# Optimization experiments

Measured on AMD Instinct MI355X. Metric: run time of the kernel, lower is better.

The kernel has to match this reference:

```python
import jax, jax.numpy as jnp
import numpy as np

K_HOPS = 4  # matches init kwarg K


def setup_inputs() -> dict:
    key = jax.random.key(0)
    ks = jax.random.split(key, 6)
    B, N, Fin, Fout = 32, 128, 64, 64
    x = jax.random.normal(ks[0], (B, N, Fin), dtype=jnp.float32)
    P = jax.random.normal(ks[1], (N, N), dtype=jnp.float32)
    Bb = jax.random.normal(ks[2], (N, 1), dtype=jnp.float32)
    Q = jax.random.normal(ks[3], (Fin, Fin), dtype=jnp.float32)
    T = jax.random.normal(ks[4], (Fin, N * Fin), dtype=jnp.float32)
    U = jax.random.normal(ks[5], (Fin, Fout), dtype=jnp.float32)
    return {"x": x, "P": P, "Bb": Bb, "Q": Q, "T": T, "U": U}


def reference(x, P, Bb, Q, T, U):
    B, N, Fin = x.shape
    # adjacency generation: O = P x + b, G = relu((O Q) T)
    O = jnp.matmul(P, x) + Bb                      # (B, N, Fin)
    G = jax.nn.relu(jnp.matmul(jnp.matmul(O, Q), T))  # (B, N, N*Fin)
    G = G.reshape(B, N, N, Fin).transpose(0, 3, 1, 2)  # (B, Fin, N, N)
    # degree normalization: A = diag(1/sqrt(colsum)) G diag(1/sqrt(rowsum))
    Dii = jnp.sqrt(jnp.sum(G, axis=-2))            # (B, Fin, N) column sums
    Djj = jnp.sqrt(jnp.sum(G, axis=-1))            # (B, Fin, N) row sums
    A = G / Dii[..., :, None] / Djj[..., None, :]  # (B, Fin, N, N)
    # K-hop power series: Asum = I + A + ... + A^{K-1}
    AA = jnp.broadcast_to(jnp.eye(N, dtype=x.dtype), A.shape)
    Asum = jnp.zeros_like(A)
    for _ in range(K_HOPS - 1):
        Asum = Asum + AA
        AA = jnp.matmul(A, AA)
    Asum = Asum + AA
    # propagate each feature channel: X[b,n,f] = sum_m Asum[b,f,n,m] x[b,m,f]
    Xf = jnp.einsum('bfnm,bmf->bnf', Asum, x)      # (B, N, Fin)
    return jnp.matmul(Xf, U)                       # (B, N, Fout)
```

## Files before the change

kernel.cpp:

```cpp
#include <hip/hip_runtime.h>


typedef __attribute__((ext_vector_type(8))) short short8v;
typedef __attribute__((ext_vector_type(4))) float f32x4;

#define WS_THE 0u
#define WS_TLE (1u << 20)
#define WS_OQH (2u << 20)
#define WS_OQL ((2u << 20) + (512u << 10))
#define WS_XFT (3u << 20)

__device__ __forceinline__ void split_bf16(float a, unsigned& hi, unsigned& lo) {
  unsigned ha = __float_as_uint(a) & 0xffff0000u;
  float d = a - __uint_as_float(ha);
  unsigned la = __float_as_uint(d) & 0xffff0000u;
  hi = ha; lo = la;
}

__global__ __launch_bounds__(256) void iag_kpre(
    const float* __restrict__ T, const float* __restrict__ x,
    const float* __restrict__ P, const float* __restrict__ Q,
    const float* __restrict__ Bb,
    unsigned short* __restrict__ The, unsigned short* __restrict__ Tle,
    unsigned short* __restrict__ OQh, unsigned short* __restrict__ OQl) {
  __shared__ __align__(16) char smem[73856];
  int bi = blockIdx.x, tid = threadIdx.x;

  if (bi < 64) {
    float* tile = (float*)smem;
    int m0 = bi * 2;
    for (int idx = tid; idx < 8192; idx += 256) {
      int k = idx >> 7, j = idx & 127;
      tile[k * 129 + j] = T[k * 8192 + m0 * 64 + j];
    }
    __syncthreads();
    int p = tid >> 1, kc = (tid & 1) * 32;
    int fj = p & 63, ml = p >> 6;
    int j = ml * 64 + fj;
    unsigned hw[16], lw[16];
#pragma unroll
    for (int kk = 0; kk < 32; kk += 2) {
      float a0 = tile[(kc + kk) * 129 + j];
      float a1 = tile[(kc + kk + 1) * 129 + j];
      unsigned h0, l0, h1, l1;
      split_bf16(a0, h0, l0);
      split_bf16(a1, h1, l1);
      hw[kk >> 1] = (h0 >> 16) | h1;
      lw[kk >> 1] = (l0 >> 16) | l1;
    }
    uint4* dh = (uint4*)(The + fj * 8192 + (m0 + ml) * 64 + kc);
    uint4* dl = (uint4*)(Tle + fj * 8192 + (m0 + ml) * 64 + kc);
#pragma unroll
    for (int i = 0; i < 4; ++i) {
      dh[i] = make_uint4(hw[4 * i], hw[4 * i + 1], hw[4 * i + 2], hw[4 * i + 3]);
      dl[i] = make_uint4(lw[4 * i], lw[4 * i + 1], lw[4 * i + 2], lw[4 * i + 3]);
    }
  } else {
    float* x_s   = (float*)smem;
    float* ptile = x_s + 128 * 64;
    float* Q_s   = ptile + 32 * 129;
    float* OcT   = Q_s + 64 * 64;
    int jb = bi - 64;
    int b = jb >> 2, r0 = (jb & 3) * 32;

    const float4* xg = (const float4*)(x + b * 8192);
    float4* xs4 = (float4*)x_s;
    for (int idx = tid; idx < 2048; idx += 256) xs4[idx] = xg[idx];
    for (int idx = tid; idx < 4096; idx += 256) {
      int nl = idx >> 7, m = idx & 127;
      ptile[nl * 129 + m] = P[(r0 + nl) * 128 + m];
    }
    const float4* qg = (const float4*)Q;
    float4* qs4 = (float4*)Q_s;
    for (int idx = tid; idx < 1024; idx += 256) qs4[idx] = qg[idx];
    __syncthreads();

    {
      int nl = tid & 31, k0 = (tid >> 5) * 8;
      float bias = Bb[r0 + nl];
      float a[8];
#pragma unroll
      for (int j = 0; j < 8; ++j) a[j] = bias;
#pragma unroll 4
      for (int m = 0; m < 128; ++m) {
        float p = ptile[nl * 129 + m];
        float4 x0 = xs4[m * 16 + (k0 >> 2)];
        float4 x1 = xs4[m * 16 + (k0 >> 2) + 1];
        a[0] += p * x0.x; a[1] += p * x0.y; a[2] += p * x0.z; a[3] += p * x0.w;
        a[4] += p * x1.x; a[5] += p * x1.y; a[6] += p * x1.z; a[7] += p * x1.w;
      }
#pragma unroll
      for (int j = 0; j < 8; ++j) OcT[(k0 + j) * 32 + nl] = a[j];
    }
    __syncthreads();
    {
      int nl = tid >> 3, j0 = (tid & 7) * 8;
      float c[8];
#pragma unroll
      for (int i = 0; i < 8; ++i) c[i] = 0.f;
      const float4* q4 = (const float4*)Q_s;
#pragma unroll 4
      for (int k = 0; k < 64; ++k) {
        float o = OcT[k * 32 + nl];
        float4 q0 = q4[k * 16 + (j0 >> 2)];
        float4 q1 = q4[k * 16 + (j0 >> 2) + 1];
        c[0] += o * q0.x; c[1] += o * q0.y; c[2] += o * q0.z; c[3] += o * q0.w;
        c[4] += o * q1.x; c[5] += o * q1.y; c[6] += o * q1.z; c[7] += o * q1.w;
      }
      unsigned hw[4], lw[4];
#pragma unroll
      for (int j = 0; j < 8; j += 2) {
        unsigned h0, l0, h1, l1;
        split_bf16(c[j], h0, l0);
        split_bf16(c[j + 1], h1, l1);
        hw[j >> 1] = (h0 >> 16) | h1;
        lw[j >> 1] = (l0 >> 16) | l1;
      }
      int n = r0 + nl;
      *(uint4*)(OQh + b * 8192 + n * 64 + j0) = make_uint4(hw[0], hw[1], hw[2], hw[3]);
      *(uint4*)(OQl + b * 8192 + n * 64 + j0) = make_uint4(lw[0], lw[1], lw[2], lw[3]);
    }
  }
}

__global__ __launch_bounds__(256, 4) void iag_k2_graph(
    const unsigned short* __restrict__ OQh, const unsigned short* __restrict__ OQl,
    const unsigned short* __restrict__ The, const unsigned short* __restrict__ Tle,
    const float* __restrict__ x, float* __restrict__ Xft) {
  __shared__ float red[4 * 128];
  __shared__ float invc[128], invr[128];
  __shared__ float wvb[2][128];
  int f = blockIdx.x, b = blockIdx.y, tid = threadIdx.x;

  if (tid < 128) wvb[0][tid] = x[b * 8192 + tid * 64 + f];

  int lane = tid & 63, w = tid >> 6;
  int li = lane & 15, lk = lane >> 4;

  const unsigned short* Abh = OQh + b * 8192;
  const unsigned short* Abl = OQl + b * 8192;
  const unsigned short* Bbh = The + f * 8192;
  const unsigned short* Bbl = Tle + f * 8192;

  short8v ah[2][2], al[2][2];
#pragma unroll
  for (int nt = 0; nt < 2; ++nt)
#pragma unroll
    for (int kh = 0; kh < 2; ++kh) {
      int off = (w * 32 + nt * 16 + li) * 64 + kh * 32 + lk * 8;
      ah[nt][kh] = *(const short8v*)(Abh + off);
      al[nt][kh] = *(const short8v*)(Abl + off);
    }

  f32x4 acc[2][8];
#pragma unroll
  for (int nt = 0; nt < 2; ++nt)
#pragma unroll
    for (int mt = 0; mt < 8; ++mt) acc[nt][mt] = (f32x4){0.f, 0.f, 0.f, 0.f};

#pragma unroll
  for (int mt = 0; mt < 8; ++mt) {
    int off = (mt * 16 + li) * 64 + lk * 8;
    short8v bh0 = *(const short8v*)(Bbh + off);
    short8v bh1 = *(const short8v*)(Bbh + off + 32);
    short8v bl0 = *(const short8v*)(Bbl + off);
    short8v bl1 = *(const short8v*)(Bbl + off + 32);
#pragma unroll
    for (int nt = 0; nt < 2; ++nt) {
      f32x4 a = acc[nt][mt];
      a = __builtin_amdgcn_mfma_f32_16x16x32_bf16(ah[nt][0], bh0, a, 0, 0, 0);
      a = __builtin_amdgcn_mfma_f32_16x16x32_bf16(ah[nt][1], bh1, a, 0, 0, 0);
      a = __builtin_amdgcn_mfma_f32_16x16x32_bf16(ah[nt][0], bl0, a, 0, 0, 0);
      a = __builtin_amdgcn_mfma_f32_16x16x32_bf16(ah[nt][1], bl1, a, 0, 0, 0);
      a = __builtin_amdgcn_mfma_f32_16x16x32_bf16(al[nt][0], bh0, a, 0, 0, 0);
      a = __builtin_amdgcn_mfma_f32_16x16x32_bf16(al[nt][1], bh1, a, 0, 0, 0);
      acc[nt][mt] = a;
    }
  }

#pragma unroll
  for (int nt = 0; nt < 2; ++nt)
#pragma unroll
    for (int mt = 0; mt < 8; ++mt)
#pragma unroll
      for (int r = 0; r < 4; ++r) acc[nt][mt][r] = fmaxf(acc[nt][mt][r], 0.f);

#pragma unroll
  for (int mt = 0; mt < 8; ++mt) {
    float cs = 0.f;
#pragma unroll
    for (int nt = 0; nt < 2; ++nt)
#pragma unroll
      for (int r = 0; r < 4; ++r) cs += acc[nt][mt][r];
    cs += __shfl_xor(cs, 16);
    cs += __shfl_xor(cs, 32);
    if (lk == 0) red[w * 128 + mt * 16 + li] = cs;
  }
  {
    float rs[2][4];
#pragma unroll
    for (int nt = 0; nt < 2; ++nt)
#pragma unroll
      for (int r = 0; r < 4; ++r) {
        float s = 0.f;
#pragma unroll
        for (int mt = 0; mt < 8; ++mt) s += acc[nt][mt][r];
        rs[nt][r] = s;
      }
#pragma unroll
    for (int d = 1; d <= 8; d <<= 1)
#pragma unroll
      for (int nt = 0; nt < 2; ++nt)
#pragma unroll
        for (int r = 0; r < 4; ++r) rs[nt][r] += __shfl_xor(rs[nt][r], d);
    if (li == 0) {
#pragma unroll
      for (int nt = 0; nt < 2; ++nt)
#pragma unroll
        for (int r = 0; r < 4; ++r)
          invr[w * 32 + nt * 16 + lk * 4 + r] = rs[nt][r];
    }
  }
  __syncthreads();
  if (tid < 128) {
    float csum = red[tid] + red[128 + tid] + red[256 + tid] + red[384 + tid];
    invc[tid] = 1.0f / sqrtf(csum);
    invr[tid] = 1.0f / sqrtf(invr[tid]);
  }
  __syncthreads();

  {
    float icf[2][4], irf[8];
#pragma unroll
    for (int nt = 0; nt < 2; ++nt)
#pragma unroll
      for (int r = 0; r < 4; ++r) icf[nt][r] = invc[w * 32 + nt * 16 + lk * 4 + r];
#pragma unroll
    for (int mt = 0; mt < 8; ++mt) irf[mt] = invr[mt * 16 + li];
#pragma unroll
    for (int nt = 0; nt < 2; ++nt)
#pragma unroll
      for (int mt = 0; mt < 8; ++mt)
#pragma unroll
        for (int r = 0; r < 4; ++r) acc[nt][mt][r] *= icf[nt][r] * irf[mt];
  }

  float sv[2][4];
#pragma unroll
  for (int nt = 0; nt < 2; ++nt)
#pragma unroll
    for (int r = 0; r < 4; ++r) sv[nt][r] = wvb[0][w * 32 + nt * 16 + lk * 4 + r];
  int cur = 0;
  for (int h = 0; h < 3; ++h) {
    float wr[8];
#pragma unroll
    for (int mt = 0; mt < 8; ++mt) wr[mt] = wvb[cur][mt * 16 + li];
    float p[2][4];
#pragma unroll
    for (int nt = 0; nt < 2; ++nt)
#pragma unroll
      for (int r = 0; r < 4; ++r) {
        float s = 0.f;
#pragma unroll
        for (int mt = 0; mt < 8; ++mt) s += acc[nt][mt][r] * wr[mt];
        p[nt][r] = s;
      }
#pragma unroll
    for (int d = 1; d <= 8; d <<= 1)
#pragma unroll
      for (int nt = 0; nt < 2; ++nt)
#pragma unroll
        for (int r = 0; r < 4; ++r) p[nt][r] += __shfl_xor(p[nt][r], d);
#pragma unroll
    for (int nt = 0; nt < 2; ++nt)
#pragma unroll
      for (int r = 0; r < 4; ++r) sv[nt][r] += p[nt][r];
    if (li == 0) {
#pragma unroll
      for (int nt = 0; nt < 2; ++nt)
#pragma unroll
        for (int r = 0; r < 4; ++r)
          wvb[cur ^ 1][w * 32 + nt * 16 + lk * 4 + r] = p[nt][r];
    }
    __syncthreads();
    cur ^= 1;
  }
  if (li == 0) {
#pragma unroll
    for (int nt = 0; nt < 2; ++nt)
#pragma unroll
      for (int r = 0; r < 4; ++r)
        Xft[(b * 64 + f) * 128 + w * 32 + nt * 16 + lk * 4 + r] = sv[nt][r];
  }
}

__global__ __launch_bounds__(256) void iag_k3_out(
    const float* __restrict__ Xft, const float* __restrict__ U,
    float* __restrict__ out) {
  __shared__ float Xf_s[64 * 36];
  __shared__ __align__(16) float U_s[64 * 64];
  int b = blockIdx.y, n0 = blockIdx.x * 32, tid = threadIdx.x;
  for (int c = tid; c < 512; c += 256) {
    int ff = c >> 3, s = c & 7;
    float4 v = *(const float4*)(Xft + (b * 64 + ff) * 128 + n0 + s * 4);
    *(float4*)(Xf_s + ff * 36 + s * 4) = v;
  }
  const float4* ug = (const float4*)U;
  float4* us = (float4*)U_s;
  for (int c = tid; c < 1024; c += 256) us[c] = ug[c];
  __syncthreads();

  int j0 = (tid & 15) * 4, nl0 = (tid >> 4) * 2;
  float a0[4] = {0.f, 0.f, 0.f, 0.f}, a1[4] = {0.f, 0.f, 0.f, 0.f};
  const float4* u4 = (const float4*)U_s;
#pragma unroll 4
  for (int ff = 0; ff < 64; ++ff) {
    float4 u = u4[ff * 16 + (j0 >> 2)];
    float xa = Xf_s[ff * 36 + nl0];
    float xb = Xf_s[ff * 36 + nl0 + 1];
    a0[0] += xa * u.x; a0[1] += xa * u.y; a0[2] += xa * u.z; a0[3] += xa * u.w;
    a1[0] += xb * u.x; a1[1] += xb * u.y; a1[2] += xb * u.z; a1[3] += xb * u.w;
  }
  *(float4*)(out + b * 8192 + (n0 + nl0) * 64 + j0) =
      make_float4(a0[0], a0[1], a0[2], a0[3]);
  *(float4*)(out + b * 8192 + (n0 + nl0 + 1) * 64 + j0) =
      make_float4(a1[0], a1[1], a1[2], a1[3]);
}

extern "C" void kernel_launch(void* const* d_in, const int* in_sizes, int n_in,
                              void* d_out, int out_size, void* d_ws, size_t ws_size,
                              hipStream_t stream) {
  const float* x  = (const float*)d_in[0];
  const float* P  = (const float*)d_in[1];
  const float* Bb = (const float*)d_in[2];
  const float* Q  = (const float*)d_in[3];
  const float* T  = (const float*)d_in[4];
  const float* U  = (const float*)d_in[5];
  char* wsb = (char*)d_ws;
  unsigned short* The = (unsigned short*)(wsb + WS_THE);
  unsigned short* Tle = (unsigned short*)(wsb + WS_TLE);
  unsigned short* OQh = (unsigned short*)(wsb + WS_OQH);
  unsigned short* OQl = (unsigned short*)(wsb + WS_OQL);
  float* Xft = (float*)(wsb + WS_XFT);

  iag_kpre<<<192, 256, 0, stream>>>(T, x, P, Q, Bb, The, Tle, OQh, OQl);
  iag_k2_graph<<<dim3(64, 32), 256, 0, stream>>>(OQh, OQl, The, Tle, x, Xft);
  iag_k3_out<<<dim3(4, 32), 256, 0, stream>>>(Xft, U, (float*)d_out);
}
```

Measured before the change: 124.2 us.

## Pre-transpose x for coalesced loads and double-buffer B fragments in graph kernel

Adds 64 extra blocks to the preprocessing kernel that transpose x per batch into a feature-major buffer. The graph kernel can then load its per-feature x vector contiguously instead of with a stride of 64 floats. The graph kernel also prefetches the next mt tile's T hi/lo fragments into a second register slot while the MFMAs for the current tile run. The occupancy hint drops from 4 to 3 blocks per CU to make room for the extra registers. The cost is one more workspace buffer, extra transpose work in the pre-kernel, and possibly lower occupancy.

Result: no change. 125.6 us (+1.1%).

```diff
diff --git a/kernel.cpp b/kernel.cpp
--- a/kernel.cpp
+++ b/kernel.cpp
@@ -9,6 +9,7 @@
 #define WS_OQH (2u << 20)
 #define WS_OQL ((2u << 20) + (512u << 10))
 #define WS_XFT (3u << 20)
+#define WS_XT  (4u << 20)
 
 __device__ __forceinline__ void split_bf16(float a, unsigned& hi, unsigned& lo) {
   unsigned ha = __float_as_uint(a) & 0xffff0000u;
@@ -22,7 +23,8 @@
     const float* __restrict__ P, const float* __restrict__ Q,
     const float* __restrict__ Bb,
     unsigned short* __restrict__ The, unsigned short* __restrict__ Tle,
-    unsigned short* __restrict__ OQh, unsigned short* __restrict__ OQl) {
+    unsigned short* __restrict__ OQh, unsigned short* __restrict__ OQl,
+    float* __restrict__ xT) {
   __shared__ __align__(16) char smem[73856];
   int bi = blockIdx.x, tid = threadIdx.x;
 
@@ -55,7 +57,7 @@
       dh[i] = make_uint4(hw[4 * i], hw[4 * i + 1], hw[4 * i + 2], hw[4 * i + 3]);
       dl[i] = make_uint4(lw[4 * i], lw[4 * i + 1], lw[4 * i + 2], lw[4 * i + 3]);
     }
-  } else {
+  } else if (bi < 192) {
     float* x_s   = (float*)smem;
     float* ptile = x_s + 128 * 64;
     float* Q_s   = ptile + 32 * 129;
@@ -120,19 +122,34 @@
       *(uint4*)(OQh + b * 8192 + n * 64 + j0) = make_uint4(hw[0], hw[1], hw[2], hw[3]);
       *(uint4*)(OQl + b * 8192 + n * 64 + j0) = make_uint4(lw[0], lw[1], lw[2], lw[3]);
     }
-  }
-}
-
-__global__ __launch_bounds__(256, 4) void iag_k2_graph(
+  } else {
+    float* tile = (float*)smem;
+    int j = bi - 192;
+    int b = j >> 1, half = j & 1;
+    const float* src = x + b * 8192 + half * 4096;
+    float* dstbase = xT + b * 8192 + half * 64;
+    for (int idx = tid; idx < 4096; idx += 256) {
+      int c = idx & 63, r = idx >> 6;
+      tile[r * 65 + c] = src[idx];
+    }
+    __syncthreads();
+    for (int idx = tid; idx < 4096; idx += 256) {
+      int r = idx & 63, c = idx >> 6;
+      dstbase[c * 128 + r] = tile[r * 65 + c];
+    }
+  }
+}
+
+__global__ __launch_bounds__(256, 3) void iag_k2_graph(
     const unsigned short* __restrict__ OQh, const unsigned short* __restrict__ OQl,
     const unsigned short* __restrict__ The, const unsigned short* __restrict__ Tle,
-    const float* __restrict__ x, float* __restrict__ Xft) {
+    const float* __restrict__ xT, float* __restrict__ Xft) {
   __shared__ float red[4 * 128];
   __shared__ float invc[128], invr[128];
   __shared__ float wvb[2][128];
   int f = blockIdx.x, b = blockIdx.y, tid = threadIdx.x;
 
-  if (tid < 128) wvb[0][tid] = x[b * 8192 + tid * 64 + f];
+  if (tid < 128) wvb[0][tid] = xT[(b * 64 + f) * 128 + tid];
 
   int lane = tid & 63, w = tid >> 6;
   int li = lane & 15, lk = lane >> 4;
@@ -158,22 +175,33 @@
 #pragma unroll
     for (int mt = 0; mt < 8; ++mt) acc[nt][mt] = (f32x4){0.f, 0.f, 0.f, 0.f};
 
+  short8v pb[2][4];
+  {
+    int off0 = li * 64 + lk * 8;
+    pb[0][0] = *(const short8v*)(Bbh + off0);
+    pb[0][1] = *(const short8v*)(Bbh + off0 + 32);
+    pb[0][2] = *(const short8v*)(Bbl + off0);
+    pb[0][3] = *(const short8v*)(Bbl + off0 + 32);
+  }
 #pragma unroll
   for (int mt = 0; mt < 8; ++mt) {
-    int off = (mt * 16 + li) * 64 + lk * 8;
-    short8v bh0 = *(const short8v*)(Bbh + off);
-    short8v bh1 = *(const short8v*)(Bbh + off + 32);
-    short8v bl0 = *(const short8v*)(Bbl + off);
-    short8v bl1 = *(const short8v*)(Bbl + off + 32);
+    int slot = mt & 1;
+    if (mt < 7) {
+      int off = ((mt + 1) * 16 + li) * 64 + lk * 8;
+      pb[slot ^ 1][0] = *(const short8v*)(Bbh + off);
+      pb[slot ^ 1][1] = *(const short8v*)(Bbh + off + 32);
+      pb[slot ^ 1][2] = *(const short8v*)(Bbl + off);
+      pb[slot ^ 1][3] = *(const short8v*)(Bbl + off + 32);
+    }
 #pragma unroll
     for (int nt = 0; nt < 2; ++nt) {
       f32x4 a = acc[nt][mt];
-      a = __builtin_amdgcn_mfma_f32_16x16x32_bf16(ah[nt][0], bh0, a, 0, 0, 0);
-      a = __builtin_amdgcn_mfma_f32_16x16x32_bf16(ah[nt][1], bh1, a, 0, 0, 0);
-      a = __builtin_amdgcn_mfma_f32_16x16x32_bf16(ah[nt][0], bl0, a, 0, 0, 0);
-      a = __builtin_amdgcn_mfma_f32_16x16x32_bf16(ah[nt][1], bl1, a, 0, 0, 0);
-      a = __builtin_amdgcn_mfma_f32_16x16x32_bf16(al[nt][0], bh0, a, 0, 0, 0);
-      a = __builtin_amdgcn_mfma_f32_16x16x32_bf16(al[nt][1], bh1, a, 0, 0, 0);
+      a = __builtin_amdgcn_mfma_f32_16x16x32_bf16(ah[nt][0], pb[slot][0], a, 0, 0, 0);
+      a = __builtin_amdgcn_mfma_f32_16x16x32_bf16(ah[nt][1], pb[slot][1], a, 0, 0, 0);
+      a = __builtin_amdgcn_mfma_f32_16x16x32_bf16(ah[nt][0], pb[slot][2], a, 0, 0, 0);
+      a = __builtin_amdgcn_mfma_f32_16x16x32_bf16(ah[nt][1], pb[slot][3], a, 0, 0, 0);
+      a = __builtin_amdgcn_mfma_f32_16x16x32_bf16(al[nt][0], pb[slot][0], a, 0, 0, 0);
+      a = __builtin_amdgcn_mfma_f32_16x16x32_bf16(al[nt][1], pb[slot][1], a, 0, 0, 0);
       acc[nt][mt] = a;
     }
   }
@@ -342,8 +370,9 @@
   unsigned short* OQh = (unsigned short*)(wsb + WS_OQH);
   unsigned short* OQl = (unsigned short*)(wsb + WS_OQL);
   float* Xft = (float*)(wsb + WS_XFT);
-
-  iag_kpre<<<192, 256, 0, stream>>>(T, x, P, Q, Bb, The, Tle, OQh, OQl);
-  iag_k2_graph<<<dim3(64, 32), 256, 0, stream>>>(OQh, OQl, The, Tle, x, Xft);
+  float* xT  = (float*)(wsb + WS_XT);
+
+  iag_kpre<<<256, 256, 0, stream>>>(T, x, P, Q, Bb, The, Tle, OQh, OQl, xT);
+  iag_k2_graph<<<dim3(64, 32), 256, 0, stream>>>(OQh, OQl, The, Tle, xT, Xft);
   iag_k3_out<<<dim3(4, 32), 256, 0, stream>>>(Xft, U, (float*)d_out);
 }
```
